# Performance work log

Hardware: AMD Instinct MI355X
Metric: run time of the kernel (lower is better)

Reference implementation:

```python
import jax, jax.numpy as jnp
import numpy as np

TOP_K = 4


def setup_inputs() -> dict:
    key = jax.random.key(0)
    ks = jax.random.split(key, 6)
    B, S, H, I, E = 2, 2048, 2880, 2880, 8
    scale = 0.02
    return {
        "x": jax.random.normal(ks[0], (B, S, H), dtype=jnp.float32),
        "router_w": jax.random.normal(ks[1], (E, H), dtype=jnp.float32) * scale,
        "router_b": jax.random.normal(ks[2], (E,), dtype=jnp.float32) * scale,
        "w_gate": jax.random.normal(ks[3], (E, H, I), dtype=jnp.float32) * scale,
        "w_up": jax.random.normal(ks[4], (E, H, I), dtype=jnp.float32) * scale,
        "w_down": jax.random.normal(ks[5], (E, I, H), dtype=jnp.float32) * scale,
    }


def _moe_forward(x, router_w, router_b, w_gate, w_up, w_down):
    B, S, H = x.shape
    E = router_w.shape[0]
    xf = x.reshape(-1, H)  # (T, H); note: self.norm is unused in the original forward
    T = xf.shape[0]

    # Router: linear -> top-k -> softmax over the k selected logits
    logits = xf @ router_w.T + router_b          # (T, E)
    topv, topi = jax.lax.top_k(logits, TOP_K)    # (T, K)
    aff_k = jax.nn.softmax(topv, axis=-1)        # (T, K), sums to 1
    aff = jnp.zeros_like(logits).at[jnp.arange(T)[:, None], topi].set(aff_k)  # (T, E)

    # Expert SwiGLU MLPs, affinity-weighted combine (aff is 0 for unselected experts)
    out = jnp.zeros_like(xf)
    for e in range(E):  # fixed small structural loop over experts
        g = xf @ w_gate[e]                       # (T, I)
        u = xf @ w_up[e]                         # (T, I)
        h = jax.nn.silu(g) * u                   # SwiGLU
        out = out + aff[:, e:e + 1] * (h @ w_down[e])
    return out.reshape(B, S, H)


def reference(x, router_w, router_b, w_gate, w_up, w_down):
    return _moe_forward(x, router_w, router_b, w_gate, w_up, w_down)
```

## Files before the change

kernel.cpp:

```cpp
#include <hip/hip_runtime.h>

#define T_TOK 4096
#define HDIM  2880
#define IDIM  2880
#define NEXP  8
#define TOPK  4
#define WEL   (2880 * 2880)

#define BM 128
#define BN 96
#define BK 64
#define NPAN 30
#define ASZ (BM * BK)
#define BSZ (BN * BK)
#define NSTEP 45

typedef __attribute__((ext_vector_type(8))) short  s16x8;
typedef __attribute__((ext_vector_type(8))) unsigned short u16x8;
typedef __attribute__((ext_vector_type(4))) float  f32x4;

__device__ __forceinline__ unsigned short f2bf(float f) {
  unsigned int u = __float_as_uint(f);
  u += 0x7FFFu + ((u >> 16) & 1u);
  return (unsigned short)(u >> 16);
}

__device__ __forceinline__ void gload16(const unsigned short* g, unsigned short* l) {
  __builtin_amdgcn_global_load_lds(
      (const __attribute__((address_space(1))) void*)g,
      (__attribute__((address_space(3))) void*)l, 16, 0, 0);
}

__global__ __launch_bounds__(256) void cvt_kernel(const float* __restrict__ x,
                                                  unsigned short* __restrict__ xb) {
  int i = blockIdx.x * 256 + threadIdx.x;
  const f32x4* p = (const f32x4*)x;
  f32x4 a = p[2 * (size_t)i];
  f32x4 b = p[2 * (size_t)i + 1];
  u16x8 o;
  o[0] = f2bf(a[0]); o[1] = f2bf(a[1]); o[2] = f2bf(a[2]); o[3] = f2bf(a[3]);
  o[4] = f2bf(b[0]); o[5] = f2bf(b[1]); o[6] = f2bf(b[2]); o[7] = f2bf(b[3]);
  *(u16x8*)(xb + (size_t)i * 8) = o;
}

__global__ __launch_bounds__(256) void transpose_group_kernel(
    const float* __restrict__ wg, const float* __restrict__ wu,
    const float* __restrict__ wd, unsigned short* __restrict__ wbuf, int ge) {
  __shared__ unsigned short st[64][72];
  const int z = blockIdx.z, j = z / 3, m = z % 3;
  const float* src = (m == 0 ? wg : (m == 1 ? wu : wd)) + (size_t)(ge + j) * WEL;
  unsigned short* dst = wbuf + (size_t)(j * 3 + m) * WEL;
  const int k0 = blockIdx.x * 64, n0 = blockIdx.y * 64;
  const int tid = threadIdx.x;
#pragma unroll
  for (int u = 0; u < 4; ++u) {
    int idx = tid + u * 256;
    int kr = idx >> 4;
    int nc = (idx & 15) * 4;
    f32x4 v = *(const f32x4*)(src + (size_t)(k0 + kr) * 2880 + (n0 + nc));
#pragma unroll
    for (int q = 0; q < 4; ++q) st[nc + q][kr] = f2bf(v[q]);
  }
  __syncthreads();
  int n = tid >> 2;
  int kc = (tid & 3) * 16;
  u16x8 a = *(const u16x8*)(&st[n][kc]);
  u16x8 b = *(const u16x8*)(&st[n][kc + 8]);
  unsigned short* po = dst + (size_t)(n0 + n) * 2880 + (k0 + kc);
  *(u16x8*)(po) = a;
  *(u16x8*)(po + 8) = b;
}

__global__ __launch_bounds__(256) void router_kernel(const float* __restrict__ x,
                                                     const float* __restrict__ rw,
                                                     const float* __restrict__ rb,
                                                     float* __restrict__ aff,
                                                     int* __restrict__ cnt,
                                                     int* __restrict__ lst) {
  const int wv = threadIdx.x >> 6, lane = threadIdx.x & 63;
  const int tok0 = (blockIdx.x * 4 + wv) * 4;
  float acc[4][NEXP];
#pragma unroll
  for (int t = 0; t < 4; ++t)
#pragma unroll
    for (int e = 0; e < NEXP; ++e) acc[t][e] = 0.f;

#pragma unroll
  for (int it = 0; it < 12; ++it) {
    int c = it * 64 + lane;
    if (c < 720) {
      f32x4 w4[NEXP];
#pragma unroll
      for (int e = 0; e < NEXP; ++e)
        w4[e] = *(const f32x4*)(rw + (size_t)e * HDIM + c * 4);
#pragma unroll
      for (int t = 0; t < 4; ++t) {
        f32x4 xv = *(const f32x4*)(x + (size_t)(tok0 + t) * HDIM + c * 4);
#pragma unroll
        for (int e = 0; e < NEXP; ++e)
          acc[t][e] += xv[0] * w4[e][0] + xv[1] * w4[e][1] + xv[2] * w4[e][2] + xv[3] * w4[e][3];
      }
    }
  }
#pragma unroll
  for (int t = 0; t < 4; ++t)
#pragma unroll
    for (int e = 0; e < NEXP; ++e) {
#pragma unroll
      for (int m = 32; m; m >>= 1) acc[t][e] += __shfl_xor(acc[t][e], m);
    }
  if (lane < 4) {
    int tok = tok0 + lane;
    float lg[NEXP];
#pragma unroll
    for (int e = 0; e < NEXP; ++e) lg[e] = acc[lane][e] + rb[e];
    bool used[NEXP];
#pragma unroll
    for (int e = 0; e < NEXP; ++e) used[e] = false;
    int bi[TOPK]; float bv[TOPK];
#pragma unroll
    for (int s = 0; s < TOPK; ++s) {
      int best = 0; float vbest = -1e30f;
#pragma unroll
      for (int e = 0; e < NEXP; ++e)
        if (!used[e] && lg[e] > vbest) { vbest = lg[e]; best = e; }
      used[best] = true; bi[s] = best; bv[s] = vbest;
    }
    float mx = bv[0];
    float w[TOPK]; float ssum = 0.f;
#pragma unroll
    for (int s = 0; s < TOPK; ++s) { w[s] = __expf(bv[s] - mx); ssum += w[s]; }
    float o[NEXP];
#pragma unroll
    for (int e = 0; e < NEXP; ++e) o[e] = 0.f;
#pragma unroll
    for (int s = 0; s < TOPK; ++s) o[bi[s]] = w[s] / ssum;
#pragma unroll
    for (int e = 0; e < NEXP; ++e) aff[(size_t)tok * NEXP + e] = o[e];
#pragma unroll
    for (int s = 0; s < TOPK; ++s) {
      int p = atomicAdd(&cnt[bi[s]], 1);
      lst[bi[s] * T_TOK + p] = tok;
    }
  }
}

__global__ void sched_kernel(const int* __restrict__ cnt, int* __restrict__ gbs,
                             int* __restrict__ ess, int* __restrict__ gtot, int G) {
  if (threadIdx.x == 0 && blockIdx.x == 0) {
    int ng = NEXP / G;
    for (int g = 0; g < ng; ++g) {
      int b = 0, s = 0;
      for (int j = 0; j < G; ++j) {
        int e = g * G + j;
        gbs[e] = b; ess[e] = s;
        b += ((cnt[e] + BM - 1) / BM) * NPAN;
        s += cnt[e];
      }
      gtot[g] = b;
    }
  }
}

__device__ __forceinline__ bool locate(int bx, const int* gbs, const int* cnts,
                                       int ge, int G, const int* gtot_g,
                                       int& e, int& m0, int& n0, int& cnt) {
  if (bx >= *gtot_g) return false;
  int j = 0;
  for (int t = 1; t < G; ++t) j += (bx >= gbs[ge + t]) ? 1 : 0;
  e = ge + j;
  cnt = cnts[e];
  int mb = (cnt + BM - 1) >> 7;
  int local = bx - gbs[e];
  int nIdx = local / mb;
  int mIdx = local - nIdx * mb;
  m0 = mIdx * BM;
  n0 = nIdx * BN;
  return true;
}

__global__ __launch_bounds__(256) void gateup_kernel(
    const unsigned short* __restrict__ xb, const unsigned short* __restrict__ wbuf,
    const float* __restrict__ aff, const int* __restrict__ lst,
    const int* __restrict__ cnts, const int* __restrict__ gbs,
    const int* __restrict__ ess, const int* __restrict__ gtot_g,
    unsigned short* __restrict__ h4, int ge, int G) {
  int e, m0, n0, cnt;
  if (!locate(blockIdx.x, gbs, cnts, ge, G, gtot_g, e, m0, n0, cnt)) return;
  const int j = e - ge;
  const int slotbase = ess[e];
  const unsigned short* wgt = wbuf + (size_t)j * 3 * WEL;
  const unsigned short* wut = wgt + WEL;

  __shared__ __align__(16) unsigned short Al[2 * ASZ];
  __shared__ __align__(16) unsigned short Bgl[2 * BSZ];
  __shared__ __align__(16) unsigned short Bul[2 * BSZ];

  const int tid = threadIdx.x;
  const int wv = tid >> 6, lane = tid & 63;
  const int msub = (wv >> 1) * 64, nsub = (wv & 1) * 48;
  const int l15 = lane & 15, l4 = lane >> 4;
  const int lr = lane >> 3, lc = lane & 7;
  const int* mylst = lst + e * T_TOK;

  const unsigned short* asrc[4]; unsigned short* adst[4];
#pragma unroll
  for (int u = 0; u < 4; ++u) {
    int s = u * 4 + wv;
    int r = s * 8 + lr;
    int tok = mylst[min(m0 + r, cnt - 1)];
    asrc[u] = xb + (size_t)tok * HDIM + (lc ^ (r & 7)) * 8;
    adst[u] = &Al[s * 512];
  }
  const unsigned short* bgsrc[3]; const unsigned short* busrc[3];
  unsigned short* bgdst[3]; unsigned short* budst[3];
#pragma unroll
  for (int u = 0; u < 3; ++u) {
    int s = u * 4 + wv;
    int r = s * 8 + lr;
    size_t off = (size_t)(n0 + r) * HDIM + (size_t)((lc ^ (r & 7)) * 8);
    bgsrc[u] = wgt + off; busrc[u] = wut + off;
    bgdst[u] = &Bgl[s * 512]; budst[u] = &Bul[s * 512];
  }

  f32x4 accg[4][3]; f32x4 accu[4][3];
#pragma unroll
  for (int mf = 0; mf < 4; ++mf)
#pragma unroll
    for (int nf = 0; nf < 3; ++nf) { accg[mf][nf] = (f32x4)0.f; accu[mf][nf] = (f32x4)0.f; }

  auto stage = [&](int buf, int k0) {
    int ao = buf * ASZ, bo = buf * BSZ;
#pragma unroll
    for (int u = 0; u < 4; ++u) gload16(asrc[u] + k0, adst[u] + ao);
#pragma unroll
    for (int u = 0; u < 3; ++u) {
      gload16(bgsrc[u] + k0, bgdst[u] + bo);
      gload16(busrc[u] + k0, budst[u] + bo);
    }
  };
  auto compute = [&](int buf) {
    const unsigned short* Ab = Al + buf * ASZ;
    const unsigned short* Bg = Bgl + buf * BSZ;
    const unsigned short* Bu = Bul + buf * BSZ;
#pragma unroll
    for (int kk = 0; kk < 2; ++kk) {
      s16x8 af[4];
#pragma unroll
      for (int mf = 0; mf < 4; ++mf) {
        int R = msub + mf * 16 + l15;
        int sl = (kk * 4 + l4) ^ (R & 7);
        af[mf] = *(const s16x8*)(&Ab[R * 64 + sl * 8]);
      }
#pragma unroll
      for (int nf = 0; nf < 3; ++nf) {
        int R = nsub + nf * 16 + l15;
        int sl = (kk * 4 + l4) ^ (R & 7);
        s16x8 bg = *(const s16x8*)(&Bg[R * 64 + sl * 8]);
        s16x8 bu = *(const s16x8*)(&Bu[R * 64 + sl * 8]);
#pragma unroll
        for (int mf = 0; mf < 4; ++mf) {
          accg[mf][nf] = __builtin_amdgcn_mfma_f32_16x16x32_bf16(af[mf], bg, accg[mf][nf], 0, 0, 0);
          accu[mf][nf] = __builtin_amdgcn_mfma_f32_16x16x32_bf16(af[mf], bu, accu[mf][nf], 0, 0, 0);
        }
      }
    }
  };

  stage(0, 0);
#pragma unroll 1
  for (int t = 0; t < NSTEP - 1; t += 2) {
    stage(1, (t + 1) * BK);
    asm volatile("s_waitcnt vmcnt(10)" ::: "memory");
    __builtin_amdgcn_s_barrier();
    compute(0);
    __builtin_amdgcn_s_barrier();
    stage(0, (t + 2) * BK);
    asm volatile("s_waitcnt vmcnt(10)" ::: "memory");
    __builtin_amdgcn_s_barrier();
    compute(1);
    __builtin_amdgcn_s_barrier();
  }
  asm volatile("s_waitcnt vmcnt(0)" ::: "memory");
  __builtin_amdgcn_s_barrier();
  compute(0);

#pragma unroll
  for (int mf = 0; mf < 4; ++mf)
#pragma unroll
    for (int r = 0; r < 4; ++r) {
      int slot = m0 + msub + mf * 16 + l4 * 4 + r;
      if (slot < cnt) {
        int tok = mylst[slot];
        float av = aff[(size_t)tok * NEXP + e];
#pragma unroll
        for (int nf = 0; nf < 3; ++nf) {
          float g = accg[mf][nf][r], uu = accu[mf][nf][r];
          float hv = (g / (1.f + __expf(-g))) * uu * av;
          int col = n0 + nsub + nf * 16 + l15;
          h4[(size_t)(slotbase + slot) * IDIM + col] = f2bf(hv);
        }
      }
    }
}

__global__ __launch_bounds__(256) void down_kernel(
    const unsigned short* __restrict__ h4, const unsigned short* __restrict__ wbuf,
    float* __restrict__ out, const int* __restrict__ lst,
    const int* __restrict__ cnts, const int* __restrict__ gbs,
    const int* __restrict__ ess, const int* __restrict__ gtot_g,
    int ge, int G) {
  int e, m0, n0, cnt;
  if (!locate(blockIdx.x, gbs, cnts, ge, G, gtot_g, e, m0, n0, cnt)) return;
  const int j = e - ge;
  const int slotbase = ess[e];
  const unsigned short* wdt = wbuf + (size_t)j * 3 * WEL + 2 * (size_t)WEL;

  __shared__ __align__(16) unsigned short Al[2 * ASZ];
  __shared__ __align__(16) unsigned short Bl[2 * BSZ];

  const int tid = threadIdx.x;
  const int wv = tid >> 6, lane = tid & 63;
  const int msub = (wv >> 1) * 64, nsub = (wv & 1) * 48;
  const int l15 = lane & 15, l4 = lane >> 4;
  const int lr = lane >> 3, lc = lane & 7;
  const int* mylst = lst + e * T_TOK;

  const unsigned short* asrc[4]; unsigned short* adst[4];
#pragma unroll
  for (int u = 0; u < 4; ++u) {
    int s = u * 4 + wv;
    int r = s * 8 + lr;
    int hr = min(m0 + r, cnt - 1);
    asrc[u] = h4 + (size_t)(slotbase + hr) * IDIM + (lc ^ (r & 7)) * 8;
    adst[u] = &Al[s * 512];
  }
  const unsigned short* bsrc[3]; unsigned short* bdst[3];
#pragma unroll
  for (int u = 0; u < 3; ++u) {
    int s = u * 4 + wv;
    int r = s * 8 + lr;
    bsrc[u] = wdt + (size_t)(n0 + r) * IDIM + (size_t)((lc ^ (r & 7)) * 8);
    bdst[u] = &Bl[s * 512];
  }

  f32x4 acc[4][3];
#pragma unroll
  for (int mf = 0; mf < 4; ++mf)
#pragma unroll
    for (int nf = 0; nf < 3; ++nf) acc[mf][nf] = (f32x4)0.f;

  auto stage = [&](int buf, int k0) {
    int ao = buf * ASZ, bo = buf * BSZ;
#pragma unroll
    for (int u = 0; u < 4; ++u) gload16(asrc[u] + k0, adst[u] + ao);
#pragma unroll
    for (int u = 0; u < 3; ++u) gload16(bsrc[u] + k0, bdst[u] + bo);
  };
  auto compute = [&](int buf) {
    const unsigned short* Ab = Al + buf * ASZ;
    const unsigned short* Bb = Bl + buf * BSZ;
#pragma unroll
    for (int kk = 0; kk < 2; ++kk) {
      s16x8 af[4];
#pragma unroll
      for (int mf = 0; mf < 4; ++mf) {
        int R = msub + mf * 16 + l15;
        int sl = (kk * 4 + l4) ^ (R & 7);
        af[mf] = *(const s16x8*)(&Ab[R * 64 + sl * 8]);
      }
#pragma unroll
      for (int nf = 0; nf < 3; ++nf) {
        int R = nsub + nf * 16 + l15;
        int sl = (kk * 4 + l4) ^ (R & 7);
        s16x8 bb = *(const s16x8*)(&Bb[R * 64 + sl * 8]);
#pragma unroll
        for (int mf = 0; mf < 4; ++mf)
          acc[mf][nf] = __builtin_amdgcn_mfma_f32_16x16x32_bf16(af[mf], bb, acc[mf][nf], 0, 0, 0);
      }
    }
  };

  stage(0, 0);
#pragma unroll 1
  for (int t = 0; t < NSTEP - 1; t += 2) {
    stage(1, (t + 1) * BK);
    asm volatile("s_waitcnt vmcnt(7)" ::: "memory");
    __builtin_amdgcn_s_barrier();
    compute(0);
    __builtin_amdgcn_s_barrier();
    stage(0, (t + 2) * BK);
    asm volatile("s_waitcnt vmcnt(7)" ::: "memory");
    __builtin_amdgcn_s_barrier();
    compute(1);
    __builtin_amdgcn_s_barrier();
  }
  asm volatile("s_waitcnt vmcnt(0)" ::: "memory");
  __builtin_amdgcn_s_barrier();
  compute(0);

#pragma unroll
  for (int mf = 0; mf < 4; ++mf)
#pragma unroll
    for (int r = 0; r < 4; ++r) {
      int slot = m0 + msub + mf * 16 + l4 * 4 + r;
      if (slot < cnt) {
        int tok = mylst[slot];
#pragma unroll
        for (int nf = 0; nf < 3; ++nf) {
          int col = n0 + nsub + nf * 16 + l15;
          atomicAdd(out + (size_t)tok * HDIM + col, acc[mf][nf][r]);
        }
      }
    }
}

extern "C" void kernel_launch(void* const* d_in, const int* in_sizes, int n_in,
                              void* d_out, int out_size, void* d_ws, size_t ws_size,
                              hipStream_t stream) {
  (void)in_sizes; (void)n_in;
  const float* x  = (const float*)d_in[0];
  const float* rw = (const float*)d_in[1];
  const float* rb = (const float*)d_in[2];
  const float* wg = (const float*)d_in[3];
  const float* wu = (const float*)d_in[4];
  const float* wd = (const float*)d_in[5];
  float* out = (float*)d_out;

  char* ws = (char*)d_ws;
  float* aff = (float*)ws;
  int*   cnt = (int*)(ws + 131072);
  int*   lst = (int*)(ws + 131584);
  int*   gbs = (int*)(ws + 262656);
  int*   ess = (int*)(ws + 262720);
  int*   gtot = (int*)(ws + 262784);
  unsigned short* xb = (unsigned short*)(ws + 263168);
  const size_t OFF_H4 = 263168 + 23592960ull;

  const size_t WELB = (size_t)WEL * 2;
  int G = 1;
  {
    size_t need8 = OFF_H4 + (size_t)16384 * IDIM * 2 + 8 * 3 * WELB;
    size_t need2 = OFF_H4 + (size_t)8192  * IDIM * 2 + 2 * 3 * WELB;
    if (ws_size >= need8) G = 8;
    else if (ws_size >= need2) G = 2;
  }
  const size_t h4b = (size_t)((G == 8) ? 16384 : (G == 2 ? 8192 : 4096)) * IDIM * 2;
  unsigned short* h4   = (unsigned short*)(ws + OFF_H4);
  unsigned short* wbuf = (unsigned short*)(ws + OFF_H4 + h4b);

  const int NG = NEXP / G;
  const int NBLK = (128 + G) * NPAN;

  hipMemsetAsync(out, 0, (size_t)out_size * sizeof(float), stream);
  hipMemsetAsync(cnt, 0, 512, stream);
  cvt_kernel<<<(T_TOK * HDIM / 8) / 256, 256, 0, stream>>>(x, xb);
  router_kernel<<<T_TOK / 16, 256, 0, stream>>>(x, rw, rb, aff, cnt, lst);
  sched_kernel<<<1, 64, 0, stream>>>(cnt, gbs, ess, gtot, G);

  for (int g = 0; g < NG; ++g) {
    int ge = g * G;
    transpose_group_kernel<<<dim3(45, 45, 3 * G), 256, 0, stream>>>(wg, wu, wd, wbuf, ge);
    gateup_kernel<<<NBLK, 256, 0, stream>>>(
        xb, wbuf, aff, lst, cnt, gbs, ess, gtot + g, h4, ge, G);
    down_kernel<<<NBLK, 256, 0, stream>>>(
        h4, wbuf, out, lst, cnt, gbs, ess, gtot + g, ge, G);
  }
}
```

Before: 1.410 ms.

## Double M tile to 256 with 8-wave blocks and XCD-aware block swizzle

```diff
diff --git a/kernel.cpp b/kernel.cpp
--- a/kernel.cpp
+++ b/kernel.cpp
@@ -7,7 +7,7 @@
 #define TOPK  4
 #define WEL   (2880 * 2880)
 
-#define BM 128
+#define BM 256
 #define BN 96
 #define BK 64
 #define NPAN 30
@@ -29,6 +29,12 @@
   __builtin_amdgcn_global_load_lds(
       (const __attribute__((address_space(1))) void*)g,
       (__attribute__((address_space(3))) void*)l, 16, 0, 0);
+}
+
+__device__ __forceinline__ int xcd_swz(int orig, int n) {
+  int q = n >> 3, r = n & 7;
+  int x = orig & 7, idx = orig >> 3;
+  return (x < r ? x * (q + 1) : r * (q + 1) + (x - r) * q) + idx;
 }
 
 __global__ __launch_bounds__(256) void cvt_kernel(const float* __restrict__ x,
@@ -170,7 +176,7 @@
   for (int t = 1; t < G; ++t) j += (bx >= gbs[ge + t]) ? 1 : 0;
   e = ge + j;
   cnt = cnts[e];
-  int mb = (cnt + BM - 1) >> 7;
+  int mb = (cnt + BM - 1) >> 8;
   int local = bx - gbs[e];
   int nIdx = local / mb;
   int mIdx = local - nIdx * mb;
@@ -179,14 +185,15 @@
   return true;
 }
 
-__global__ __launch_bounds__(256) void gateup_kernel(
+__global__ __launch_bounds__(512) void gateup_kernel(
     const unsigned short* __restrict__ xb, const unsigned short* __restrict__ wbuf,
     const float* __restrict__ aff, const int* __restrict__ lst,
     const int* __restrict__ cnts, const int* __restrict__ gbs,
     const int* __restrict__ ess, const int* __restrict__ gtot_g,
     unsigned short* __restrict__ h4, int ge, int G) {
   int e, m0, n0, cnt;
-  if (!locate(blockIdx.x, gbs, cnts, ge, G, gtot_g, e, m0, n0, cnt)) return;
+  const int bx = xcd_swz(blockIdx.x, gridDim.x);
+  if (!locate(bx, gbs, cnts, ge, G, gtot_g, e, m0, n0, cnt)) return;
   const int j = e - ge;
   const int slotbase = ess[e];
   const unsigned short* wgt = wbuf + (size_t)j * 3 * WEL;
@@ -206,21 +213,24 @@
   const unsigned short* asrc[4]; unsigned short* adst[4];
 #pragma unroll
   for (int u = 0; u < 4; ++u) {
-    int s = u * 4 + wv;
+    int s = wv + 8 * u;
     int r = s * 8 + lr;
     int tok = mylst[min(m0 + r, cnt - 1)];
     asrc[u] = xb + (size_t)tok * HDIM + (lc ^ (r & 7)) * 8;
     adst[u] = &Al[s * 512];
   }
-  const unsigned short* bgsrc[3]; const unsigned short* busrc[3];
-  unsigned short* bgdst[3]; unsigned short* budst[3];
-#pragma unroll
-  for (int u = 0; u < 3; ++u) {
-    int s = u * 4 + wv;
-    int r = s * 8 + lr;
-    size_t off = (size_t)(n0 + r) * HDIM + (size_t)((lc ^ (r & 7)) * 8);
-    bgsrc[u] = wgt + off; busrc[u] = wut + off;
-    bgdst[u] = &Bgl[s * 512]; budst[u] = &Bul[s * 512];
+  const int sBx = (wv < 4) ? (8 + wv) : (4 + wv);
+  const unsigned short* bgsrc0; const unsigned short* busrc0; const unsigned short* bxsrc;
+  unsigned short* bgdst0; unsigned short* budst0; unsigned short* bxdst;
+  {
+    int r0 = wv * 8 + lr;
+    size_t o0 = (size_t)(n0 + r0) * HDIM + (size_t)((lc ^ (r0 & 7)) * 8);
+    bgsrc0 = wgt + o0; bgdst0 = &Bgl[wv * 512];
+    busrc0 = wut + o0; budst0 = &Bul[wv * 512];
+    int rx = sBx * 8 + lr;
+    size_t ox = (size_t)(n0 + rx) * HDIM + (size_t)((lc ^ (rx & 7)) * 8);
+    bxsrc = (wv < 4) ? (wgt + ox) : (wut + ox);
+    bxdst = (wv < 4) ? &Bgl[sBx * 512] : &Bul[sBx * 512];
   }
 
   f32x4 accg[4][3]; f32x4 accu[4][3];
@@ -233,11 +243,9 @@
     int ao = buf * ASZ, bo = buf * BSZ;
 #pragma unroll
     for (int u = 0; u < 4; ++u) gload16(asrc[u] + k0, adst[u] + ao);
-#pragma unroll
-    for (int u = 0; u < 3; ++u) {
-      gload16(bgsrc[u] + k0, bgdst[u] + bo);
-      gload16(busrc[u] + k0, budst[u] + bo);
-    }
+    gload16(bgsrc0 + k0, bgdst0 + bo);
+    gload16(busrc0 + k0, budst0 + bo);
+    gload16(bxsrc + k0, bxdst + bo);
   };
   auto compute = [&](int buf) {
     const unsigned short* Ab = Al + buf * ASZ;
@@ -271,12 +279,12 @@
 #pragma unroll 1
   for (int t = 0; t < NSTEP - 1; t += 2) {
     stage(1, (t + 1) * BK);
-    asm volatile("s_waitcnt vmcnt(10)" ::: "memory");
+    asm volatile("s_waitcnt vmcnt(7)" ::: "memory");
     __builtin_amdgcn_s_barrier();
     compute(0);
     __builtin_amdgcn_s_barrier();
     stage(0, (t + 2) * BK);
-    asm volatile("s_waitcnt vmcnt(10)" ::: "memory");
+    asm volatile("s_waitcnt vmcnt(7)" ::: "memory");
     __builtin_amdgcn_s_barrier();
     compute(1);
     __builtin_amdgcn_s_barrier();
@@ -304,14 +312,15 @@
     }
 }
 
-__global__ __launch_bounds__(256) void down_kernel(
+__global__ __launch_bounds__(512) void down_kernel(
     const unsigned short* __restrict__ h4, const unsigned short* __restrict__ wbuf,
     float* __restrict__ out, const int* __restrict__ lst,
     const int* __restrict__ cnts, const int* __restrict__ gbs,
     const int* __restrict__ ess, const int* __restrict__ gtot_g,
     int ge, int G) {
   int e, m0, n0, cnt;
-  if (!locate(blockIdx.x, gbs, cnts, ge, G, gtot_g, e, m0, n0, cnt)) return;
+  const int bx = xcd_swz(blockIdx.x, gridDim.x);
+  if (!locate(bx, gbs, cnts, ge, G, gtot_g, e, m0, n0, cnt)) return;
   const int j = e - ge;
   const int slotbase = ess[e];
   const unsigned short* wdt = wbuf + (size_t)j * 3 * WEL + 2 * (size_t)WEL;
@@ -329,19 +338,23 @@
   const unsigned short* asrc[4]; unsigned short* adst[4];
 #pragma unroll
   for (int u = 0; u < 4; ++u) {
-    int s = u * 4 + wv;
+    int s = wv + 8 * u;
     int r = s * 8 + lr;
     int hr = min(m0 + r, cnt - 1);
     asrc[u] = h4 + (size_t)(slotbase + hr) * IDIM + (lc ^ (r & 7)) * 8;
     adst[u] = &Al[s * 512];
   }
-  const unsigned short* bsrc[3]; unsigned short* bdst[3];
-#pragma unroll
-  for (int u = 0; u < 3; ++u) {
-    int s = u * 4 + wv;
-    int r = s * 8 + lr;
-    bsrc[u] = wdt + (size_t)(n0 + r) * IDIM + (size_t)((lc ^ (r & 7)) * 8);
-    bdst[u] = &Bl[s * 512];
+  const unsigned short* bsrc0; unsigned short* bdst0;
+  const unsigned short* bsrc1 = nullptr; unsigned short* bdst1 = nullptr;
+  {
+    int r0 = wv * 8 + lr;
+    bsrc0 = wdt + (size_t)(n0 + r0) * IDIM + (size_t)((lc ^ (r0 & 7)) * 8);
+    bdst0 = &Bl[wv * 512];
+    if (wv < 4) {
+      int r1 = (8 + wv) * 8 + lr;
+      bsrc1 = wdt + (size_t)(n0 + r1) * IDIM + (size_t)((lc ^ (r1 & 7)) * 8);
+      bdst1 = &Bl[(8 + wv) * 512];
+    }
   }
 
   f32x4 acc[4][3];
@@ -354,8 +367,12 @@
     int ao = buf * ASZ, bo = buf * BSZ;
 #pragma unroll
     for (int u = 0; u < 4; ++u) gload16(asrc[u] + k0, adst[u] + ao);
-#pragma unroll
-    for (int u = 0; u < 3; ++u) gload16(bsrc[u] + k0, bdst[u] + bo);
+    gload16(bsrc0 + k0, bdst0 + bo);
+    if (wv < 4) gload16(bsrc1 + k0, bdst1 + bo);
+  };
+  auto waitprev = [&]() {
+    if (wv < 4) { asm volatile("s_waitcnt vmcnt(6)" ::: "memory"); }
+    else        { asm volatile("s_waitcnt vmcnt(5)" ::: "memory"); }
   };
   auto compute = [&](int buf) {
     const unsigned short* Ab = Al + buf * ASZ;
@@ -385,12 +402,12 @@
 #pragma unroll 1
   for (int t = 0; t < NSTEP - 1; t += 2) {
     stage(1, (t + 1) * BK);
-    asm volatile("s_waitcnt vmcnt(7)" ::: "memory");
+    waitprev();
     __builtin_amdgcn_s_barrier();
     compute(0);
     __builtin_amdgcn_s_barrier();
     stage(0, (t + 2) * BK);
-    asm volatile("s_waitcnt vmcnt(7)" ::: "memory");
+    waitprev();
     __builtin_amdgcn_s_barrier();
     compute(1);
     __builtin_amdgcn_s_barrier();
@@ -450,7 +467,7 @@
   unsigned short* wbuf = (unsigned short*)(ws + OFF_H4 + h4b);
 
   const int NG = NEXP / G;
-  const int NBLK = (128 + G) * NPAN;
+  const int NBLK = (T_TOK * TOPK / BM + NEXP) * NPAN;
 
   hipMemsetAsync(out, 0, (size_t)out_size * sizeof(float), stream);
   hipMemsetAsync(cnt, 0, 512, stream);
@@ -461,9 +478,9 @@
   for (int g = 0; g < NG; ++g) {
     int ge = g * G;
     transpose_group_kernel<<<dim3(45, 45, 3 * G), 256, 0, stream>>>(wg, wu, wd, wbuf, ge);
-    gateup_kernel<<<NBLK, 256, 0, stream>>>(
+    gateup_kernel<<<NBLK, 512, 0, stream>>>(
         xb, wbuf, aff, lst, cnt, gbs, ess, gtot + g, h4, ge, G);
-    down_kernel<<<NBLK, 256, 0, stream>>>(
+    down_kernel<<<NBLK, 512, 0, stream>>>(
         h4, wbuf, out, lst, cnt, gbs, ess, gtot + g, ge, G);
   }
 }
```

Measured after the change: 1.676 ms. +18.9%, slower.
